# Kernel optimization log

Measured on AMD Instinct MI355X. Metric: run time of the kernel, lower is better.

The kernel has to match this reference:

```python
import jax, jax.numpy as jnp
import numpy as np

N, D, V, T = 2048, 64, 32000, 512
K_WTA = 256
X_DECAY, U_DECAY = 0.97, 0.97
SPIKE_RATE = 0.01
FORGET_ETA = 0.01
HOMEO_TAU = 1.0
GAMMA_MAX = 1.0


def ln_row(z, eps=1e-6):
    # torch .std is unbiased (ddof=1)
    m = z.mean(-1, keepdims=True)
    s = z.std(-1, ddof=1, keepdims=True)
    return (z - m) / (s + eps)


def setup_inputs() -> dict:
    key = jax.random.key(0)
    ks = jax.random.split(key, 6)
    return {
        "tokens": jax.random.randint(ks[0], (T,), 0, V),
        "spike_u": jax.random.uniform(ks[1], (T, N), dtype=jnp.float32),
        "E": jax.random.normal(ks[2], (D, N), dtype=jnp.float32) / np.sqrt(N).astype(np.float32),
        "Dx": jax.random.normal(ks[3], (N, D), dtype=jnp.float32) / np.sqrt(D).astype(np.float32),
        "Dy": jax.random.normal(ks[4], (N, D), dtype=jnp.float32) / np.sqrt(D).astype(np.float32),
        "token_emb": jax.random.normal(ks[5], (V, D), dtype=jnp.float32) / np.sqrt(D).astype(np.float32),
    }


def reference(tokens, spike_u, E, Dx, Dy, token_emb):
    def step(carry, inp):
        x, rho = carry
        tok, u = inp
        v_prev = token_emb[tok]                                   # (D,)
        x_t = X_DECAY * x + jax.nn.relu(Dx @ v_prev)              # (N,)
        x_t = x_t / (jnp.sum(jnp.abs(x_t)) + 1e-6)                # L1 normalize
        a_hat = ln_row(rho @ x_t)                                 # (D,) ln_before_Dy
        # branches=4 with elementwise softplus == softplus on full matvec
        y_core = jax.nn.softplus(Dy @ a_hat)                      # (N,)
        y_core = y_core + (u < SPIKE_RATE).astype(y_core.dtype)   # spike noise
        # k-WTA: keep top K_WTA entries
        _, idx = jax.lax.top_k(y_core, K_WTA)
        mask = jnp.zeros((N,), bool).at[idx].set(True)
        y_core = y_core * mask.astype(y_core.dtype)
        y_t = jax.nn.relu(y_core) * jax.nn.relu(x_t)
        # homeostasis (torch uses .item() -> constant scale)
        s = y_t.sum()
        scale = jnp.where(s > 1e-8, jnp.minimum(1.0, HOMEO_TAU / (s + 1e-8)), 1.0)
        y_t = y_t * jax.lax.stop_gradient(scale)
        v_star = ln_row(E @ y_t)                                  # (D,)
        # surprisal gain (torch uses .item() -> constant)
        p = jax.nn.softmax(v_star)
        H = -(p * jnp.log(p + 1e-12)).sum()
        gain = jnp.minimum(GAMMA_MAX, H / jnp.log(jnp.float32(D) + 1e-6) * GAMMA_MAX)
        gain = jax.lax.stop_gradient(gain)
        # dynamic top-k on x_t via rank masking (jit-safe data-dependent k)
        k_dyn = jnp.clip((N * (0.05 + 0.25 * gain)).astype(jnp.int32), 1, N)
        order = jnp.argsort(-x_t)
        ranks = jnp.zeros((N,), jnp.int32).at[order].set(jnp.arange(N, dtype=jnp.int32))
        x_t = x_t * (ranks < k_dyn).astype(x_t.dtype)
        # local forgetting on inactive columns, then Hebbian update
        inactive = (x_t <= 0).astype(rho.dtype)
        rho = rho * (1.0 - FORGET_ETA * inactive[None, :])
        rho = U_DECAY * (rho + gain * jnp.outer(v_prev, x_t))
        return (x_t, rho), v_star

    init = (jnp.zeros((N,), jnp.float32), jnp.zeros((D, N), jnp.float32))
    (_, _), v_stack = jax.lax.scan(step, init, (tokens, spike_u))
    return v_stack  # (T, D)
```

## Files before the change

kernel.cpp:

```cpp
#include <hip/hip_runtime.h>
#include <math.h>

#define NB   32
#define NTH  256
#define CH   64
#define NN   2048
#define DD   64
#define TT   512
#define KWTA 256
#define PAD  65

__device__ __align__(16) double g_L1[2][NB];
__device__ __align__(16) double g_r [2][NB][DD];
__device__ __align__(16) double g_s [2][NB];
__device__ __align__(16) double g_e [2][NB][DD];
__device__ __align__(16) float  g_xg[2][NN];
__device__ __align__(16) float  g_yg[2][NN];
__device__ unsigned g_bar;

__global__ void bdh_init() { if (threadIdx.x == 0) g_bar = 0u; }

__device__ __forceinline__ void grid_barrier(unsigned& epoch) {
  __syncthreads();
  if (threadIdx.x == 0) {
    epoch += 1u;
    __threadfence();
    __hip_atomic_fetch_add(&g_bar, 1u, __ATOMIC_RELAXED, __HIP_MEMORY_SCOPE_AGENT);
    const unsigned target = epoch * (unsigned)NB;
    while (__hip_atomic_load(&g_bar, __ATOMIC_RELAXED, __HIP_MEMORY_SCOPE_AGENT) < target)
      __builtin_amdgcn_s_sleep(1);
    __builtin_amdgcn_fence(__ATOMIC_ACQUIRE, "agent");
  }
  __syncthreads();
}

__device__ void select_topk(const unsigned* __restrict__ keys, int K, int n0, int tid,
                            float* __restrict__ keep,
                            unsigned* __restrict__ hist,
                            unsigned* __restrict__ wsum,
                            int* __restrict__ misc)
{
  const int wave = tid >> 6, lane = tid & 63;
  const int sub = tid & 7;
  uint4* h4 = (uint4*)hist;
  unsigned prefix = 0u, pmask = 0u;
  int remK = K;
  for (int lev = 0; lev < 4; ++lev) {
    const int shf = 24 - 8*lev;
    const uint4 z = {0u,0u,0u,0u};
    h4[tid] = z; h4[tid + 256] = z;
    __syncthreads();
    #pragma unroll
    for (int j = 0; j < 8; ++j)
      if ((keys[j] & pmask) == prefix)
        atomicAdd(&hist[(((keys[j] >> shf) & 255u) << 3) + sub], 1u);
    __syncthreads();
    const uint4 a = h4[tid*2], bq = h4[tid*2 + 1];
    const unsigned c = a.x+a.y+a.z+a.w + bq.x+bq.y+bq.z+bq.w;
    unsigned s = c;
    #pragma unroll
    for (int off = 1; off < 64; off <<= 1) {
      unsigned o = __shfl_down(s, off, 64);
      if (lane + off < 64) s += o;
    }
    if (lane == 0) wsum[wave] = s;
    __syncthreads();
    unsigned hi = 0;
    for (int w = wave + 1; w < 4; ++w) hi += wsum[w];
    const unsigned A = s + hi;
    if (A >= (unsigned)remK && (A - c) < (unsigned)remK) {
      misc[0] = tid;
      misc[1] = remK - (int)(A - c);
    }
    __syncthreads();
    prefix |= ((unsigned)misc[0]) << shf;
    pmask  |= (255u << shf);
    remK = misc[1];
  }
  const unsigned thr = prefix;
  const unsigned R = (unsigned)remK;
  int lc[8]; int cnt = 0;
  #pragma unroll
  for (int j = 0; j < 8; ++j) { lc[j] = cnt; cnt += (keys[j] == thr) ? 1 : 0; }
  unsigned e = (unsigned)cnt;
  #pragma unroll
  for (int off = 1; off < 64; off <<= 1) {
    unsigned o = __shfl_up(e, off, 64);
    if (lane >= off) e += o;
  }
  if (lane == 63) wsum[4 + wave] = e;
  __syncthreads();
  unsigned base = 0;
  for (int w = 0; w < wave; ++w) base += wsum[4 + w];
  const unsigned excl = base + e - (unsigned)cnt;
  #pragma unroll
  for (int j = 0; j < 8; ++j) {
    const int g = tid*8 + j;
    const unsigned gg = (unsigned)(g - n0);
    if (gg < (unsigned)CH) {
      const bool kp = (keys[j] > thr) || ((keys[j] == thr) && (excl + (unsigned)lc[j] < R));
      keep[gg] = kp ? 1.0f : 0.0f;
    }
  }
  __syncthreads();
}

__global__ void __launch_bounds__(NTH)
bdh_main(const int* __restrict__ tokens, const float* __restrict__ spike_u,
         const float* __restrict__ Emat, const float* __restrict__ Dx,
         const float* __restrict__ Dy, const float* __restrict__ temb,
         float* __restrict__ out)
{
  __shared__ float sh_rho[DD][PAD];
  __shared__ float sh_Dx[CH][PAD];
  __shared__ float sh_Dy[CH][PAD];
  __shared__ float sh_E [DD][PAD];
  __shared__ int   sh_tok[TT];
  __shared__ float sh_v[2][DD];
  __shared__ float sh_xstate[CH];
  __shared__ float sh_xtun[CH];
  __shared__ float sh_xt[CH];
  __shared__ float sh_y[CH];
  __shared__ float sh_yt[CH];
  __shared__ float sh_ahat[DD];
  __shared__ float sh_keep[CH];
  __shared__ float sh_ffac[CH];
  __shared__ unsigned sh_hist[256*8];
  __shared__ unsigned sh_wsum[8];
  __shared__ int sh_misc[4];
  __shared__ float sh_fmisc[4];
  __shared__ double sh_dred[8];
  __shared__ double sh_rd[4][DD];

  const int tid = threadIdx.x;
  const int b   = blockIdx.x;
  const int n0  = b * CH;
  const int i4  = tid >> 2;
  const int p4  = tid & 3;
  const int lane = tid & 63;
  const int wv   = tid >> 6;
  unsigned epoch = 0u;

  for (int k = tid; k < TT; k += NTH) sh_tok[k] = tokens[k];
  for (int k = tid; k < DD*PAD; k += NTH) (&sh_rho[0][0])[k] = 0.0f;
  if (tid < CH) sh_xstate[tid] = 0.0f;
  for (int r = wv; r < CH; r += 4) {
    sh_Dx[r][lane] = Dx[(size_t)(n0 + r)*DD + lane];
    sh_Dy[r][lane] = Dy[(size_t)(n0 + r)*DD + lane];
    sh_E [r][lane] = Emat[(size_t)r*NN + n0 + lane];
  }
  __syncthreads();
  if (tid < DD) sh_v[0][tid] = temb[(size_t)sh_tok[0]*DD + tid];
  __syncthreads();

  for (int t = 0; t < TT; ++t) {
    const int par = t & 1;

    const float spu = spike_u[(size_t)t*NN + n0 + i4];
    if (t + 1 < TT && tid < DD)
      sh_v[(t + 1) & 1][tid] = temb[(size_t)sh_tok[t + 1]*DD + tid];

    float d1 = 0.0f;
    {
      const float* dxr = &sh_Dx[i4][p4*16];
      const float* vv  = &sh_v[par][p4*16];
      #pragma unroll
      for (int j = 0; j < 16; ++j) d1 += dxr[j] * vv[j];
    }
    d1 += __shfl_xor(d1, 1, 64);
    d1 += __shfl_xor(d1, 2, 64);
    float xnew = 0.0f;
    if (p4 == 0) {
      xnew = 0.97f * sh_xstate[i4] + fmaxf(d1, 0.0f);
      sh_xtun[i4] = xnew;
    }
    {
      double v = (p4 == 0) ? (double)fabsf(xnew) : 0.0;
      #pragma unroll
      for (int off = 32; off > 0; off >>= 1) v += __shfl_xor(v, off, 64);
      if (lane == 0) sh_dred[wv] = v;
      __syncthreads();
      if (tid == 0) g_L1[par][b] = sh_dred[0] + sh_dred[1] + sh_dred[2] + sh_dred[3];
    }
    float qa = 0.0f;
    {
      const float* rr = &sh_rho[i4][p4*16];
      const float* xx = &sh_xtun[p4*16];
      #pragma unroll
      for (int j = 0; j < 16; ++j) qa += rr[j] * xx[j];
    }
    qa += __shfl_xor(qa, 1, 64);
    qa += __shfl_xor(qa, 2, 64);
    if (p4 == 0) g_r[par][b][i4] = (double)qa;
    grid_barrier(epoch);

    {
      double acc = 0.0;
      #pragma unroll
      for (int j = 0; j < 8; ++j) acc += g_r[par][wv*8 + j][lane];
      sh_rd[wv][lane] = acc;
    }
    {
      double v = (tid < NB) ? g_L1[par][tid] : 0.0;
      if (tid < 64) {
        #pragma unroll
        for (int off = 32; off > 0; off >>= 1) v += __shfl_xor(v, off, 64);
        if (tid == 0) sh_dred[0] = v;
      }
    }
    __syncthreads();
    const float Lden = (float)sh_dred[0] + 1e-6f;
    if (tid < DD) {
      const double qd = sh_rd[0][tid] + sh_rd[1][tid] + sh_rd[2][tid] + sh_rd[3][tid];
      const float rf = (float)qd / Lden;
      float s1 = rf;
      #pragma unroll
      for (int off = 32; off > 0; off >>= 1) s1 += __shfl_xor(s1, off, 64);
      const float m = s1 * (1.0f/64.0f);
      const float dv = rf - m;
      float s2 = dv * dv;
      #pragma unroll
      for (int off = 32; off > 0; off >>= 1) s2 += __shfl_xor(s2, off, 64);
      const float sd = sqrtf(s2 * (1.0f/63.0f));
      sh_ahat[tid] = dv / (sd + 1e-6f);
      const float xv = sh_xtun[tid] / Lden;
      sh_xt[tid] = xv;
      g_xg[par][n0 + tid] = xv;
    }
    __syncthreads();
    float d2 = 0.0f;
    {
      const float* dyr = &sh_Dy[i4][p4*16];
      const float* aa  = &sh_ahat[p4*16];
      #pragma unroll
      for (int j = 0; j < 16; ++j) d2 += dyr[j] * aa[j];
    }
    d2 += __shfl_xor(d2, 1, 64);
    d2 += __shfl_xor(d2, 2, 64);
    if (p4 == 0) {
      const float sp = fmaxf(d2, 0.0f) + log1pf(expf(-fabsf(d2)));
      const float y  = sp + ((spu < 0.01f) ? 1.0f : 0.0f);
      sh_y[i4] = y;
      g_yg[par][n0 + i4] = y;
    }
    grid_barrier(epoch);

    unsigned ykeys[8], xkeys[8];
    {
      const float4* py = ((const float4*)g_yg[par]) + tid*2;
      const float4* px = ((const float4*)g_xg[par]) + tid*2;
      float4 y0 = py[0], y1 = py[1];
      float4 x0 = px[0], x1 = px[1];
      ykeys[0]=__float_as_uint(y0.x); ykeys[1]=__float_as_uint(y0.y);
      ykeys[2]=__float_as_uint(y0.z); ykeys[3]=__float_as_uint(y0.w);
      ykeys[4]=__float_as_uint(y1.x); ykeys[5]=__float_as_uint(y1.y);
      ykeys[6]=__float_as_uint(y1.z); ykeys[7]=__float_as_uint(y1.w);
      xkeys[0]=__float_as_uint(x0.x); xkeys[1]=__float_as_uint(x0.y);
      xkeys[2]=__float_as_uint(x0.z); xkeys[3]=__float_as_uint(x0.w);
      xkeys[4]=__float_as_uint(x1.x); xkeys[5]=__float_as_uint(x1.y);
      xkeys[6]=__float_as_uint(x1.z); xkeys[7]=__float_as_uint(x1.w);
    }
    select_topk(ykeys, KWTA, n0, tid, sh_keep, sh_hist, sh_wsum, sh_misc);
    if (tid < CH) {
      const float ym = sh_keep[tid] * sh_y[tid];
      sh_yt[tid] = fmaxf(ym, 0.0f) * fmaxf(sh_xt[tid], 0.0f);
    }
    __syncthreads();
    float eacc = 0.0f;
    {
      const float* er = &sh_E[i4][p4*16];
      const float* yy = &sh_yt[p4*16];
      #pragma unroll
      for (int j = 0; j < 16; ++j) eacc += er[j] * yy[j];
    }
    eacc += __shfl_xor(eacc, 1, 64);
    eacc += __shfl_xor(eacc, 2, 64);
    if (p4 == 0) g_e[par][b][i4] = (double)eacc;
    {
      double v = (tid < CH) ? (double)sh_yt[tid] : 0.0;
      #pragma unroll
      for (int off = 32; off > 0; off >>= 1) v += __shfl_xor(v, off, 64);
      if (lane == 0) sh_dred[4 + wv] = v;
      __syncthreads();
      if (tid == 0) g_s[par][b] = sh_dred[4] + sh_dred[5] + sh_dred[6] + sh_dred[7];
    }
    grid_barrier(epoch);

    {
      double acc = 0.0;
      #pragma unroll
      for (int j = 0; j < 8; ++j) acc += g_e[par][wv*8 + j][lane];
      sh_rd[wv][lane] = acc;
    }
    {
      double v = (tid < NB) ? g_s[par][tid] : 0.0;
      if (tid < 64) {
        #pragma unroll
        for (int off = 32; off > 0; off >>= 1) v += __shfl_xor(v, off, 64);
        if (tid == 0) sh_dred[0] = v;
      }
    }
    __syncthreads();
    const float sf = (float)sh_dred[0];
    const float scale = (sf > 1e-8f) ? fminf(1.0f, 1.0f/(sf + 1e-8f)) : 1.0f;
    if (tid < DD) {
      const double ed = sh_rd[0][tid] + sh_rd[1][tid] + sh_rd[2][tid] + sh_rd[3][tid];
      const float z = scale * (float)ed;
      float s1 = z;
      #pragma unroll
      for (int off = 32; off > 0; off >>= 1) s1 += __shfl_xor(s1, off, 64);
      const float m = s1 * (1.0f/64.0f);
      const float dv = z - m;
      float s2 = dv * dv;
      #pragma unroll
      for (int off = 32; off > 0; off >>= 1) s2 += __shfl_xor(s2, off, 64);
      const float sd = sqrtf(s2 * (1.0f/63.0f));
      const float vs = dv / (sd + 1e-6f);
      if (b == 0) out[t*DD + tid] = vs;
      float mx = vs;
      #pragma unroll
      for (int off = 32; off > 0; off >>= 1) mx = fmaxf(mx, __shfl_xor(mx, off, 64));
      const float ex = expf(vs - mx);
      float se = ex;
      #pragma unroll
      for (int off = 32; off > 0; off >>= 1) se += __shfl_xor(se, off, 64);
      const float pp = ex / se;
      float ht = -pp * logf(pp + 1e-12f);
      #pragma unroll
      for (int off = 32; off > 0; off >>= 1) ht += __shfl_xor(ht, off, 64);
      if (tid == 0) sh_fmisc[0] = fminf(1.0f, ht / logf(64.0f));
    }
    __syncthreads();
    const float gain = sh_fmisc[0];
    int kd = (int)(2048.0f * (0.05f + 0.25f * gain));
    kd = kd < 1 ? 1 : (kd > NN ? NN : kd);
    select_topk(xkeys, kd, n0, tid, sh_keep, sh_hist, sh_wsum, sh_misc);
    if (tid < CH) {
      const float xm = sh_keep[tid] * sh_xt[tid];
      sh_xstate[tid] = xm;
      sh_ffac[tid] = (xm <= 0.0f) ? (1.0f - 0.01f) : 1.0f;
    }
    __syncthreads();
    {
      const float vd = sh_v[par][i4];
      float* rr = &sh_rho[i4][p4*16];
      const float* xx = &sh_xstate[p4*16];
      const float* ff = &sh_ffac[p4*16];
      #pragma unroll
      for (int j = 0; j < 16; ++j)
        rr[j] = 0.97f * (rr[j]*ff[j] + gain * (vd * xx[j]));
    }
    __syncthreads();
  }
}

extern "C" void kernel_launch(void* const* d_in, const int* in_sizes, int n_in,
                              void* d_out, int out_size, void* d_ws, size_t ws_size,
                              hipStream_t stream) {
  const int*   tokens = (const int*)d_in[0];
  const float* spike  = (const float*)d_in[1];
  const float* Emat   = (const float*)d_in[2];
  const float* Dx     = (const float*)d_in[3];
  const float* Dy     = (const float*)d_in[4];
  const float* temb   = (const float*)d_in[5];
  float* out = (float*)d_out;
  (void)in_sizes; (void)n_in; (void)out_size; (void)d_ws; (void)ws_size;
  bdh_init<<<dim3(1), dim3(64), 0, stream>>>();
  bdh_main<<<dim3(NB), dim3(NTH), 0, stream>>>(tokens, spike, Emat, Dx, Dy, temb, out);
}
```

Measured before the change: 11.34 ms.

## Halve block count and replace atomic-counter grid barrier with per-block flags

Switches from 32 to 16 persistent blocks, each owning 128 columns, so fewer blocks take part in each of the three per-step grid barriers. The shared counter barrier is replaced by per-block padded flags that one wave polls in parallel, aiming to remove atomic contention on a single counter. Cross-block partial sums are exchanged as float instead of double, and the parity double-buffering of global scratch is dropped. The trade-off is twice the per-block matvec and rho-update work. Reusing the same scratch buffers every step could also introduce a race if a fast block overwrites them before a slow block has read them.

```diff
diff --git a/kernel.cpp b/kernel.cpp
--- a/kernel.cpp
+++ b/kernel.cpp
@@ -1,37 +1,58 @@
 #include <hip/hip_runtime.h>
 #include <math.h>
 
-#define NB   32
+#define NB   16
 #define NTH  256
-#define CH   64
+#define CH   128
 #define NN   2048
 #define DD   64
 #define TT   512
 #define KWTA 256
-#define PAD  65
-
-__device__ __align__(16) double g_L1[2][NB];
-__device__ __align__(16) double g_r [2][NB][DD];
-__device__ __align__(16) double g_s [2][NB];
-__device__ __align__(16) double g_e [2][NB][DD];
-__device__ __align__(16) float  g_xg[2][NN];
-__device__ __align__(16) float  g_yg[2][NN];
-__device__ unsigned g_bar;
-
-__global__ void bdh_init() { if (threadIdx.x == 0) g_bar = 0u; }
+#define PA   65
+#define PB   132
+
+struct __align__(128) BarFlag { unsigned v; unsigned pad[31]; };
+__device__ BarFlag g_flag[NB];
+__device__ __align__(16) float  g_rf[NB][DD];
+__device__ __align__(16) float  g_ef[NB][DD];
+__device__ __align__(16) double g_L1[NB];
+__device__ __align__(16) double g_s [NB];
+__device__ __align__(16) float  g_xg[NN];
+__device__ __align__(16) float  g_yg[NN];
+
+__global__ void bdh_init() { if (threadIdx.x < NB) g_flag[threadIdx.x].v = 0u; }
 
 __device__ __forceinline__ void grid_barrier(unsigned& epoch) {
-  __syncthreads();
-  if (threadIdx.x == 0) {
-    epoch += 1u;
-    __threadfence();
-    __hip_atomic_fetch_add(&g_bar, 1u, __ATOMIC_RELAXED, __HIP_MEMORY_SCOPE_AGENT);
-    const unsigned target = epoch * (unsigned)NB;
-    while (__hip_atomic_load(&g_bar, __ATOMIC_RELAXED, __HIP_MEMORY_SCOPE_AGENT) < target)
+  epoch += 1u;
+  __syncthreads();
+  if (threadIdx.x < 64) {
+    if (threadIdx.x == 0) {
+      __threadfence();
+      __hip_atomic_store(&g_flag[blockIdx.x].v, epoch, __ATOMIC_RELAXED,
+                         __HIP_MEMORY_SCOPE_AGENT);
+    }
+    const int i = (int)threadIdx.x;
+    for (;;) {
+      const bool ok = (i >= NB) ||
+        (__hip_atomic_load(&g_flag[i].v, __ATOMIC_RELAXED,
+                           __HIP_MEMORY_SCOPE_AGENT) >= epoch);
+      if (__all(ok)) break;
       __builtin_amdgcn_s_sleep(1);
+    }
     __builtin_amdgcn_fence(__ATOMIC_ACQUIRE, "agent");
   }
   __syncthreads();
+}
+
+__device__ __forceinline__ double wredd(double v) {
+  #pragma unroll
+  for (int off = 32; off > 0; off >>= 1) v += __shfl_xor(v, off, 64);
+  return v;
+}
+__device__ __forceinline__ float wredf(float v) {
+  #pragma unroll
+  for (int off = 32; off > 0; off >>= 1) v += __shfl_xor(v, off, 64);
+  return v;
 }
 
 __device__ void select_topk(const unsigned* __restrict__ keys, int K, int n0, int tid,
@@ -111,10 +132,10 @@
          const float* __restrict__ Dy, const float* __restrict__ temb,
          float* __restrict__ out)
 {
-  __shared__ float sh_rho[DD][PAD];
-  __shared__ float sh_Dx[CH][PAD];
-  __shared__ float sh_Dy[CH][PAD];
-  __shared__ float sh_E [DD][PAD];
+  __shared__ float sh_rho[DD][PB];
+  __shared__ float sh_Dx[CH][PA];
+  __shared__ float sh_Dy[CH][PA];
+  __shared__ float sh_E [DD][PB];
   __shared__ int   sh_tok[TT];
   __shared__ float sh_v[2][DD];
   __shared__ float sh_xstate[CH];
@@ -132,22 +153,27 @@
   __shared__ double sh_dred[8];
   __shared__ double sh_rd[4][DD];
 
-  const int tid = threadIdx.x;
-  const int b   = blockIdx.x;
-  const int n0  = b * CH;
-  const int i4  = tid >> 2;
-  const int p4  = tid & 3;
+  const int tid  = threadIdx.x;
+  const int b    = blockIdx.x;
+  const int n0   = b * CH;
+  const int i2   = tid >> 1;
+  const int p2   = tid & 1;
+  const int d4   = tid >> 2;
+  const int p4   = tid & 3;
   const int lane = tid & 63;
   const int wv   = tid >> 6;
   unsigned epoch = 0u;
 
   for (int k = tid; k < TT; k += NTH) sh_tok[k] = tokens[k];
-  for (int k = tid; k < DD*PAD; k += NTH) (&sh_rho[0][0])[k] = 0.0f;
+  for (int k = tid; k < DD*PB; k += NTH) (&sh_rho[0][0])[k] = 0.0f;
   if (tid < CH) sh_xstate[tid] = 0.0f;
   for (int r = wv; r < CH; r += 4) {
     sh_Dx[r][lane] = Dx[(size_t)(n0 + r)*DD + lane];
     sh_Dy[r][lane] = Dy[(size_t)(n0 + r)*DD + lane];
-    sh_E [r][lane] = Emat[(size_t)r*NN + n0 + lane];
+  }
+  for (int r = wv; r < DD; r += 4) {
+    sh_E[r][lane]      = Emat[(size_t)r*NN + n0 + lane];
+    sh_E[r][lane + 64] = Emat[(size_t)r*NN + n0 + lane + 64];
   }
   __syncthreads();
   if (tid < DD) sh_v[0][tid] = temb[(size_t)sh_tok[0]*DD + tid];
@@ -156,99 +182,89 @@
   for (int t = 0; t < TT; ++t) {
     const int par = t & 1;
 
-    const float spu = spike_u[(size_t)t*NN + n0 + i4];
+    float spu = 0.0f;
+    if (p2 == 0) spu = spike_u[(size_t)t*NN + n0 + i2];
     if (t + 1 < TT && tid < DD)
-      sh_v[(t + 1) & 1][tid] = temb[(size_t)sh_tok[t + 1]*DD + tid];
+      sh_v[par ^ 1][tid] = temb[(size_t)sh_tok[t + 1]*DD + tid];
 
     float d1 = 0.0f;
     {
-      const float* dxr = &sh_Dx[i4][p4*16];
-      const float* vv  = &sh_v[par][p4*16];
-      #pragma unroll
-      for (int j = 0; j < 16; ++j) d1 += dxr[j] * vv[j];
+      const float* dxr = &sh_Dx[i2][p2*32];
+      const float* vv  = &sh_v[par][p2*32];
+      #pragma unroll
+      for (int j = 0; j < 32; ++j) d1 += dxr[j] * vv[j];
     }
     d1 += __shfl_xor(d1, 1, 64);
-    d1 += __shfl_xor(d1, 2, 64);
     float xnew = 0.0f;
-    if (p4 == 0) {
-      xnew = 0.97f * sh_xstate[i4] + fmaxf(d1, 0.0f);
-      sh_xtun[i4] = xnew;
-    }
-    {
-      double v = (p4 == 0) ? (double)fabsf(xnew) : 0.0;
-      #pragma unroll
-      for (int off = 32; off > 0; off >>= 1) v += __shfl_xor(v, off, 64);
+    if (p2 == 0) {
+      xnew = 0.97f * sh_xstate[i2] + fmaxf(d1, 0.0f);
+      sh_xtun[i2] = xnew;
+    }
+    {
+      double v = (p2 == 0) ? (double)fabsf(xnew) : 0.0;
+      v = wredd(v);
       if (lane == 0) sh_dred[wv] = v;
       __syncthreads();
-      if (tid == 0) g_L1[par][b] = sh_dred[0] + sh_dred[1] + sh_dred[2] + sh_dred[3];
+      if (tid == 0) g_L1[b] = sh_dred[0] + sh_dred[1] + sh_dred[2] + sh_dred[3];
     }
     float qa = 0.0f;
     {
-      const float* rr = &sh_rho[i4][p4*16];
-      const float* xx = &sh_xtun[p4*16];
-      #pragma unroll
-      for (int j = 0; j < 16; ++j) qa += rr[j] * xx[j];
+      const float* rr = &sh_rho[d4][0];
+      #pragma unroll
+      for (int j = 0; j < 32; ++j) { const int c = p4 + 4*j; qa += rr[c] * sh_xtun[c]; }
     }
     qa += __shfl_xor(qa, 1, 64);
     qa += __shfl_xor(qa, 2, 64);
-    if (p4 == 0) g_r[par][b][i4] = (double)qa;
+    if (p4 == 0) g_rf[b][d4] = qa;
     grid_barrier(epoch);
 
     {
       double acc = 0.0;
       #pragma unroll
-      for (int j = 0; j < 8; ++j) acc += g_r[par][wv*8 + j][lane];
+      for (int j = 0; j < 4; ++j) acc += (double)g_rf[(wv<<2) + j][lane];
       sh_rd[wv][lane] = acc;
     }
-    {
-      double v = (tid < NB) ? g_L1[par][tid] : 0.0;
-      if (tid < 64) {
-        #pragma unroll
-        for (int off = 32; off > 0; off >>= 1) v += __shfl_xor(v, off, 64);
-        if (tid == 0) sh_dred[0] = v;
-      }
+    if (tid < 64) {
+      double v = (tid < NB) ? g_L1[tid] : 0.0;
+      v = wredd(v);
+      if (tid == 0) sh_dred[0] = v;
     }
     __syncthreads();
     const float Lden = (float)sh_dred[0] + 1e-6f;
-    if (tid < DD) {
+    if (tid < 64) {
       const double qd = sh_rd[0][tid] + sh_rd[1][tid] + sh_rd[2][tid] + sh_rd[3][tid];
       const float rf = (float)qd / Lden;
-      float s1 = rf;
-      #pragma unroll
-      for (int off = 32; off > 0; off >>= 1) s1 += __shfl_xor(s1, off, 64);
-      const float m = s1 * (1.0f/64.0f);
+      const float m  = wredf(rf) * (1.0f/64.0f);
       const float dv = rf - m;
-      float s2 = dv * dv;
-      #pragma unroll
-      for (int off = 32; off > 0; off >>= 1) s2 += __shfl_xor(s2, off, 64);
-      const float sd = sqrtf(s2 * (1.0f/63.0f));
+      const float sd = sqrtf(wredf(dv*dv) * (1.0f/63.0f));
       sh_ahat[tid] = dv / (sd + 1e-6f);
-      const float xv = sh_xtun[tid] / Lden;
-      sh_xt[tid] = xv;
-      g_xg[par][n0 + tid] = xv;
+    } else if (tid < 192) {
+      const int l = tid - 64;
+      const float xv = sh_xtun[l] / Lden;
+      sh_xt[l] = xv;
+      g_xg[n0 + l] = xv;
     }
     __syncthreads();
     float d2 = 0.0f;
     {
-      const float* dyr = &sh_Dy[i4][p4*16];
-      const float* aa  = &sh_ahat[p4*16];
-      #pragma unroll
-      for (int j = 0; j < 16; ++j) d2 += dyr[j] * aa[j];
+      const float* dyr = &sh_Dy[i2][p2*32];
+      const float* aa  = &sh_ahat[p2*32];
+      #pragma unroll
+      for (int j = 0; j < 32; ++j) d2 += dyr[j] * aa[j];
     }
     d2 += __shfl_xor(d2, 1, 64);
-    d2 += __shfl_xor(d2, 2, 64);
-    if (p4 == 0) {
+    if (p2 == 0) {
       const float sp = fmaxf(d2, 0.0f) + log1pf(expf(-fabsf(d2)));
       const float y  = sp + ((spu < 0.01f) ? 1.0f : 0.0f);
-      sh_y[i4] = y;
-      g_yg[par][n0 + i4] = y;
+      sh_y[i2] = y;
+      g_yg[n0 + i2] = y;
     }
     grid_barrier(epoch);
 
     unsigned ykeys[8], xkeys[8];
     {
-      const float4* py = ((const float4*)g_yg[par]) + tid*2;
-      const float4* px = ((const float4*)g_xg[par]) + tid*2;
+      const float4* py = ((const float4*)g_yg) + tid*2;
+      const float4* px = ((const float4*)g_xg) + tid*2;
       float4 y0 = py[0], y1 = py[1];
       float4 x0 = px[0], x1 = px[1];
       ykeys[0]=__float_as_uint(y0.x); ykeys[1]=__float_as_uint(y0.y);
@@ -266,68 +282,53 @@
       sh_yt[tid] = fmaxf(ym, 0.0f) * fmaxf(sh_xt[tid], 0.0f);
     }
     __syncthreads();
-    float eacc = 0.0f;
-    {
-      const float* er = &sh_E[i4][p4*16];
-      const float* yy = &sh_yt[p4*16];
-      #pragma unroll
-      for (int j = 0; j < 16; ++j) eacc += er[j] * yy[j];
-    }
-    eacc += __shfl_xor(eacc, 1, 64);
-    eacc += __shfl_xor(eacc, 2, 64);
-    if (p4 == 0) g_e[par][b][i4] = (double)eacc;
+    float ea = 0.0f;
+    {
+      const float* er = &sh_E[d4][0];
+      #pragma unroll
+      for (int j = 0; j < 32; ++j) { const int c = p4 + 4*j; ea += er[c] * sh_yt[c]; }
+    }
+    ea += __shfl_xor(ea, 1, 64);
+    ea += __shfl_xor(ea, 2, 64);
+    if (p4 == 0) g_ef[b][d4] = ea;
     {
       double v = (tid < CH) ? (double)sh_yt[tid] : 0.0;
-      #pragma unroll
-      for (int off = 32; off > 0; off >>= 1) v += __shfl_xor(v, off, 64);
+      v = wredd(v);
       if (lane == 0) sh_dred[4 + wv] = v;
       __syncthreads();
-      if (tid == 0) g_s[par][b] = sh_dred[4] + sh_dred[5] + sh_dred[6] + sh_dred[7];
+      if (tid == 0) g_s[b] = sh_dred[4] + sh_dred[5] + sh_dred[6] + sh_dred[7];
     }
     grid_barrier(epoch);
 
     {
       double acc = 0.0;
       #pragma unroll
-      for (int j = 0; j < 8; ++j) acc += g_e[par][wv*8 + j][lane];
+      for (int j = 0; j < 4; ++j) acc += (double)g_ef[(wv<<2) + j][lane];
       sh_rd[wv][lane] = acc;
     }
-    {
-      double v = (tid < NB) ? g_s[par][tid] : 0.0;
-      if (tid < 64) {
-        #pragma unroll
-        for (int off = 32; off > 0; off >>= 1) v += __shfl_xor(v, off, 64);
-        if (tid == 0) sh_dred[0] = v;
-      }
+    if (tid < 64) {
+      double v = (tid < NB) ? g_s[tid] : 0.0;
+      v = wredd(v);
+      if (tid == 0) sh_dred[0] = v;
     }
     __syncthreads();
     const float sf = (float)sh_dred[0];
     const float scale = (sf > 1e-8f) ? fminf(1.0f, 1.0f/(sf + 1e-8f)) : 1.0f;
-    if (tid < DD) {
+    if (tid < 64) {
       const double ed = sh_rd[0][tid] + sh_rd[1][tid] + sh_rd[2][tid] + sh_rd[3][tid];
       const float z = scale * (float)ed;
-      float s1 = z;
-      #pragma unroll
-      for (int off = 32; off > 0; off >>= 1) s1 += __shfl_xor(s1, off, 64);
-      const float m = s1 * (1.0f/64.0f);
+      const float m  = wredf(z) * (1.0f/64.0f);
       const float dv = z - m;
-      float s2 = dv * dv;
-      #pragma unroll
-      for (int off = 32; off > 0; off >>= 1) s2 += __shfl_xor(s2, off, 64);
-      const float sd = sqrtf(s2 * (1.0f/63.0f));
+      const float sd = sqrtf(wredf(dv*dv) * (1.0f/63.0f));
       const float vs = dv / (sd + 1e-6f);
       if (b == 0) out[t*DD + tid] = vs;
       float mx = vs;
       #pragma unroll
       for (int off = 32; off > 0; off >>= 1) mx = fmaxf(mx, __shfl_xor(mx, off, 64));
       const float ex = expf(vs - mx);
-      float se = ex;
-      #pragma unroll
-      for (int off = 32; off > 0; off >>= 1) se += __shfl_xor(se, off, 64);
+      const float se = wredf(ex);
       const float pp = ex / se;
-      float ht = -pp * logf(pp + 1e-12f);
-      #pragma unroll
-      for (int off = 32; off > 0; off >>= 1) ht += __shfl_xor(ht, off, 64);
+      const float ht = wredf(-pp * logf(pp + 1e-12f));
       if (tid == 0) sh_fmisc[0] = fminf(1.0f, ht / logf(64.0f));
     }
     __syncthreads();
@@ -342,13 +343,13 @@
     }
     __syncthreads();
     {
-      const float vd = sh_v[par][i4];
-      float* rr = &sh_rho[i4][p4*16];
-      const float* xx = &sh_xstate[p4*16];
-      const float* ff = &sh_ffac[p4*16];
-      #pragma unroll
-      for (int j = 0; j < 16; ++j)
-        rr[j] = 0.97f * (rr[j]*ff[j] + gain * (vd * xx[j]));
+      const float vd = sh_v[par][d4];
+      float* rr = &sh_rho[d4][0];
+      #pragma unroll
+      for (int j = 0; j < 32; ++j) {
+        const int c = p4 + 4*j;
+        rr[c] = 0.97f * (rr[c]*sh_ffac[c] + gain * (vd * sh_xstate[c]));
+      }
     }
     __syncthreads();
   }
```

After: 9.784 ms. -13.7%, faster.
